# Kernel tuning notes

Hardware: AMD Instinct MI355X
Metric: run time of the kernel (lower is better)

Reference implementation:

```python
import jax, jax.numpy as jnp
import numpy as np

N = 50000      # nodes
IN = 128       # in_channels
H = 2          # heads
C = 64         # hidden_channels (per head)
E = 800000     # edges (before self-loops)
OUT = 40       # out_channels
BN_EPS = 1e-5
NEG_SLOPE = 0.2  # PyG GATConv default


def _bn(x, g, b):
    # BatchNorm1d forward with batch statistics (training-mode math, biased var)
    mu = jnp.mean(x, axis=0)
    v = jnp.var(x, axis=0)
    return (x - mu) * jax.lax.rsqrt(v + BN_EPS) * g + b


def _gat_conv(x, src, dst, W, a_src, a_dst, bias, concat):
    n = x.shape[0]
    h = (x @ W).reshape(n, H, C)                      # [N,H,C] per-head projection
    al_s = jnp.einsum('nhc,hc->nh', h, a_src)         # [N,H]
    al_d = jnp.einsum('nhc,hc->nh', h, a_dst)
    e = jax.nn.leaky_relu(al_s[src] + al_d[dst], NEG_SLOPE)  # [E,H]
    # segment softmax over edges sharing the same destination
    m = jax.ops.segment_max(e, dst, num_segments=n)
    ex = jnp.exp(e - m[dst])
    s = jax.ops.segment_sum(ex, dst, num_segments=n)
    alpha = ex / s[dst]                               # [E,H]
    out = jax.ops.segment_sum(h[src] * alpha[..., None], dst, num_segments=n)  # [N,H,C]
    out = out.reshape(n, H * C) if concat else out.mean(axis=1)
    return out + bias


def setup_inputs() -> dict:
    key = jax.random.key(0)
    ks = jax.random.split(key, 16)
    g = lambda k, shp, scale=1.0: jax.random.normal(k, shp, dtype=jnp.float32) * scale
    x = g(ks[0], (N, IN))
    edge_index = jax.random.randint(ks[1], (2, E), 0, N, dtype=jnp.int32)
    s = 1.0 / np.sqrt(IN)
    s2 = 1.0 / np.sqrt(H * C)
    return {
        'x': x,
        'edge_index': edge_index,
        'bn0_g': jnp.ones((IN,), jnp.float32), 'bn0_b': jnp.zeros((IN,), jnp.float32),
        'W1': g(ks[2], (IN, H * C), s), 'a1_src': g(ks[3], (H, C), s), 'a1_dst': g(ks[4], (H, C), s),
        'b1': jnp.zeros((H * C,), jnp.float32),
        'bn1_g': jnp.ones((H * C,), jnp.float32), 'bn1_b': jnp.zeros((H * C,), jnp.float32),
        'W2': g(ks[5], (H * C, H * C), s2), 'a2_src': g(ks[6], (H, C), s2), 'a2_dst': g(ks[7], (H, C), s2),
        'b2': jnp.zeros((C,), jnp.float32),
        'bn2_g': jnp.ones((C,), jnp.float32), 'bn2_b': jnp.zeros((C,), jnp.float32),
        'Wf': g(ks[8], (C, OUT), 1.0 / np.sqrt(C)), 'bf': jnp.zeros((OUT,), jnp.float32),
    }


def reference(x, edge_index, bn0_g, bn0_b, W1, a1_src, a1_dst, b1, bn1_g, bn1_b,
              W2, a2_src, a2_dst, b2, bn2_g, bn2_b, Wf, bf):
    n = x.shape[0]
    loop = jnp.arange(n, dtype=edge_index.dtype)
    src = jnp.concatenate([edge_index[0], loop])  # add self-loops (PyG default)
    dst = jnp.concatenate([edge_index[1], loop])
    h = _bn(x, bn0_g, bn0_b)
    # layer 1: concat heads
    h = _gat_conv(h, src, dst, W1, a1_src, a1_dst, b1, concat=True)
    h = jax.nn.elu(_bn(h, bn1_g, bn1_b))
    # (dropout is identity in eval mode)
    # layer 2: average heads
    h = _gat_conv(h, src, dst, W2, a2_src, a2_dst, b2, concat=False)
    h = jax.nn.elu(_bn(h, bn2_g, bn2_b))
    return h @ Wf + bf
```

## Files before the change

kernel.cpp:

```cpp
#include <hip/hip_runtime.h>
#include <hip/hip_fp16.h>


#define NEG_SLOPE 0.2f
#define BN_EPS 1e-5f

typedef short bf16x8 __attribute__((ext_vector_type(8)));
typedef float f32x4 __attribute__((ext_vector_type(4)));

static __device__ __forceinline__ unsigned short f2bf(float f) {
    union { float f; unsigned u; } v; v.f = f;
    unsigned r = v.u + 0x7FFF + ((v.u >> 16) & 1);
    return (unsigned short)(r >> 16);
}
static __device__ __forceinline__ float2 bf2x2(unsigned v) {
    union { unsigned u; float f; } a, b;
    a.u = v << 16; b.u = v & 0xffff0000u;
    return make_float2(a.f, b.f);
}
static __device__ __forceinline__ float halfsel(unsigned p, int head) {
    __half2 h = *(__half2*)&p;
    return head ? __high2float(h) : __low2float(h);
}

template <int C>
static __device__ __forceinline__ void d_bnstat(const float* __restrict__ x, int M,
                                                int rowsPerBlock, float* __restrict__ sums,
                                                int b, float* red) {
    constexpr int TPR = C / 4;
    constexpr int RS  = 256 / TPR;
    const int t = threadIdx.x;
    const int cg = t % TPR, rg = t / TPR, w = t >> 6, lane = t & 63;
    int r0 = b * rowsPerBlock + rg;
    int r1 = min(M, b * rowsPerBlock + rowsPerBlock);
    float4 s = make_float4(0, 0, 0, 0), q = make_float4(0, 0, 0, 0);
    #pragma unroll 4
    for (int r = r0; r < r1; r += RS) {
        float4 v = *(const float4*)&x[(size_t)r * C + cg * 4];
        s.x += v.x; s.y += v.y; s.z += v.z; s.w += v.w;
        q.x += v.x * v.x; q.y += v.y * v.y; q.z += v.z * v.z; q.w += v.w * v.w;
    }
    #pragma unroll
    for (int off = TPR; off < 64; off <<= 1) {
        s.x += __shfl_xor(s.x, off); s.y += __shfl_xor(s.y, off);
        s.z += __shfl_xor(s.z, off); s.w += __shfl_xor(s.w, off);
        q.x += __shfl_xor(q.x, off); q.y += __shfl_xor(q.y, off);
        q.z += __shfl_xor(q.z, off); q.w += __shfl_xor(q.w, off);
    }
    if (lane < TPR) {
        *(float4*)&red[w * 2 * C + cg * 4] = s;
        *(float4*)&red[w * 2 * C + C + cg * 4] = q;
    }
    __syncthreads();
    for (int idx = t; idx < 2 * C; idx += 256) {
        float tot = red[idx] + red[2 * C + idx] + red[4 * C + idx] + red[6 * C + idx];
        atomicAdd(&sums[idx], tot);
    }
}

template <int C>
__global__ __launch_bounds__(256) void k_bnstat2(const float* __restrict__ x, int M,
                                                 int rowsPerBlock, float* __restrict__ sums) {
    __shared__ __align__(16) float red[4 * 2 * C];
    d_bnstat<C>(x, M, rowsPerBlock, sums, blockIdx.x, red);
}

__global__ __launch_bounds__(256) void k_prep(
    const int* __restrict__ ei, int E, int rgrid,
    const float* __restrict__ x, int M, int bgrid,
    const float* __restrict__ W1, const float* __restrict__ W2,
    int* __restrict__ cnt, unsigned short* __restrict__ rank,
    float* __restrict__ sums,
    unsigned short* __restrict__ wt1, unsigned short* __restrict__ wt2) {
    __shared__ __align__(16) float red[4 * 2 * 128];
    int b = blockIdx.x;
    if (b < rgrid) {
        int i = b * 256 + threadIdx.x;
        if (i < E) {
            int d = ei[E + i];
            rank[i] = (unsigned short)atomicAdd(&cnt[d], 1);
        }
    } else if (b < rgrid + bgrid) {
        d_bnstat<128>(x, M, 256, sums, b - rgrid, red);
    } else {
        int idx = (b - rgrid - bgrid) * 256 + threadIdx.x;
        if (idx < 128 * 128) {
            int n = idx >> 7, k = idx & 127;
            wt1[idx] = f2bf(W1[k * 128 + n]);
            wt2[idx] = f2bf(W2[k * 128 + n]);
        }
    }
}

__global__ __launch_bounds__(256) void k_scan(const int* __restrict__ cnt, int Nn,
                                              int* __restrict__ gcur,
                                              int* __restrict__ rowptr,
                                              unsigned short* __restrict__ degs) {
    __shared__ int wsum[4];
    __shared__ int s_base;
    int t = threadIdx.x, lane = t & 63, w = t >> 6;
    int i = blockIdx.x * 256 + t;
    int v = (i < Nn) ? cnt[i] + 1 : 0;
    int x = v;
    #pragma unroll
    for (int off = 1; off < 64; off <<= 1) {
        int y = __shfl_up(x, off);
        if (lane >= off) x += y;
    }
    if (lane == 63) wsum[w] = x;
    __syncthreads();
    if (t < 4) {
        int val = wsum[t];
        int xs = val;
        #pragma unroll
        for (int off = 1; off < 4; off <<= 1) {
            int y = __shfl_up(xs, off);
            if (t >= off) xs += y;
        }
        if (t == 3) s_base = atomicAdd(gcur, xs);
        wsum[t] = xs - val;
    }
    __syncthreads();
    if (i < Nn) {
        rowptr[i] = s_base + wsum[w] + (x - v);
        degs[i] = (unsigned short)v;
    }
}

static __device__ __forceinline__ void d_fill(int b, const int* __restrict__ ei,
                                              const unsigned short* __restrict__ rank,
                                              const int* __restrict__ rowptr, int E, int Nn,
                                              unsigned short* __restrict__ ssrc) {
    int i = b * 256 + threadIdx.x;
    if (i < E) {
        int s = ei[i], d = ei[E + i];
        ssrc[rowptr[d] + 1 + (int)rank[i]] = (unsigned short)s;
    } else if (i < E + Nn) {
        int d = i - E;
        ssrc[rowptr[d]] = (unsigned short)d;
    }
}

static __device__ __forceinline__ void d_mfma(
    int blk, const float* __restrict__ A, const unsigned short* __restrict__ wt,
    const float* __restrict__ sums, const float* __restrict__ bng, const float* __restrict__ bnb,
    int elu, const float* __restrict__ asrc, const float* __restrict__ adst, int M,
    unsigned short* __restrict__ hb, float* __restrict__ als, float* __restrict__ ald) {
    __shared__ unsigned short As[64 * 136];
    __shared__ __align__(16) float stl[256];
    const int t = threadIdx.x;
    const int w = t >> 6, lane = t & 63;
    const int c = lane & 15, q = lane >> 4;
    const int row0 = blk * 64;

    if (t < 128) {
        float mu = sums[t] / (float)M;
        float var = sums[128 + t] / (float)M - mu * mu;
        float s = bng[t] * rsqrtf(var + BN_EPS);
        stl[t] = s;
        stl[128 + t] = bnb[t] - mu * s;
    }
    __syncthreads();

    const int gr = row0 + w * 16 + c;
    const bool rok = gr < M;

    float4 av[4][2];
    #pragma unroll
    for (int ks = 0; ks < 4; ks++) {
        const int cc = (ks * 4 + q) * 8;
        #pragma unroll
        for (int h = 0; h < 2; h++)
            av[ks][h] = rok ? *(const float4*)&A[(size_t)gr * 128 + cc + h * 4]
                            : make_float4(0.f, 0.f, 0.f, 0.f);
    }

    bf16x8 af[4];
    #pragma unroll
    for (int ks = 0; ks < 4; ks++) {
        const int cc = (ks * 4 + q) * 8;
        union { bf16x8 v; unsigned u[4]; } pk;
        #pragma unroll
        for (int h = 0; h < 2; h++) {
            float4 v = av[ks][h];
            if (rok) {
                float4 sc = *(const float4*)&stl[cc + h * 4];
                float4 sh = *(const float4*)&stl[128 + cc + h * 4];
                v.x = v.x * sc.x + sh.x; v.y = v.y * sc.y + sh.y;
                v.z = v.z * sc.z + sh.z; v.w = v.w * sc.w + sh.w;
                if (elu) {
                    v.x = v.x > 0.f ? v.x : expm1f(v.x);
                    v.y = v.y > 0.f ? v.y : expm1f(v.y);
                    v.z = v.z > 0.f ? v.z : expm1f(v.z);
                    v.w = v.w > 0.f ? v.w : expm1f(v.w);
                }
            }
            pk.u[h * 2]     = ((unsigned)f2bf(v.y) << 16) | f2bf(v.x);
            pk.u[h * 2 + 1] = ((unsigned)f2bf(v.w) << 16) | f2bf(v.z);
        }
        af[ks] = pk.v;
    }

    f32x4 acc[8] = {};
    #pragma unroll
    for (int half = 0; half < 2; half++) {
        bf16x8 br[8][2];
        #pragma unroll
        for (int tl = 0; tl < 8; tl++) {
            #pragma unroll
            for (int kk = 0; kk < 2; kk++)
                br[tl][kk] = *(const bf16x8*)&wt[(size_t)(tl * 16 + c) * 128 + ((half * 2 + kk) * 4 + q) * 8];
        }
        #pragma unroll
        for (int kk = 0; kk < 2; kk++) {
            #pragma unroll
            for (int tl = 0; tl < 8; tl++)
                acc[tl] = __builtin_amdgcn_mfma_f32_16x16x32_bf16(af[half * 2 + kk], br[tl][kk], acc[tl], 0, 0, 0);
        }
    }

    float as_[8], ad_[8];
    #pragma unroll
    for (int tl = 0; tl < 8; tl++) { as_[tl] = asrc[tl * 16 + c]; ad_[tl] = adst[tl * 16 + c]; }
    #pragma unroll
    for (int reg = 0; reg < 4; reg++) {
        float s0 = 0.f, s1 = 0.f, d0 = 0.f, d1 = 0.f;
        #pragma unroll
        for (int tl = 0; tl < 4; tl++) { s0 += acc[tl][reg] * as_[tl]; d0 += acc[tl][reg] * ad_[tl]; }
        #pragma unroll
        for (int tl = 4; tl < 8; tl++) { s1 += acc[tl][reg] * as_[tl]; d1 += acc[tl][reg] * ad_[tl]; }
        #pragma unroll
        for (int off = 1; off < 16; off <<= 1) {
            s0 += __shfl_xor(s0, off); s1 += __shfl_xor(s1, off);
            d0 += __shfl_xor(d0, off); d1 += __shfl_xor(d1, off);
        }
        int grow = row0 + w * 16 + q * 4 + reg;
        if (c == 0 && grow < M) {
            *(float2*)&als[(size_t)grow * 2] = make_float2(s0, s1);
            *(float2*)&ald[(size_t)grow * 2] = make_float2(d0, d1);
        }
    }

    #pragma unroll
    for (int reg = 0; reg < 4; reg++) {
        #pragma unroll
        for (int tl = 0; tl < 8; tl++)
            As[(w * 16 + q * 4 + reg) * 136 + tl * 16 + c] = f2bf(acc[tl][reg]);
    }
    #pragma unroll
    for (int j = 0; j < 4; j++) {
        int f = j * 64 + lane;
        int r = f >> 4, ch = f & 15;
        int grow = row0 + w * 16 + r;
        if (grow < M) {
            uint4 v = *(uint4*)&As[(w * 16 + r) * 136 + ch * 8];
            *(uint4*)&hb[(size_t)grow * 128 + ch * 8] = v;
        }
    }
}

__global__ __launch_bounds__(256) void k_mfma(
    const float* __restrict__ A, const unsigned short* __restrict__ wt,
    const float* __restrict__ sums, const float* __restrict__ bng, const float* __restrict__ bnb,
    int elu, const float* __restrict__ asrc, const float* __restrict__ adst, int M,
    unsigned short* __restrict__ hb, float* __restrict__ als, float* __restrict__ ald) {
    d_mfma(blockIdx.x, A, wt, sums, bng, bnb, elu, asrc, adst, M, hb, als, ald);
}

__global__ __launch_bounds__(256) void k_fill_mfma(
    const float* __restrict__ A, const unsigned short* __restrict__ wt,
    const float* __restrict__ sums, const float* __restrict__ bng, const float* __restrict__ bnb,
    const float* __restrict__ asrc, const float* __restrict__ adst, int M, int ggrid,
    unsigned short* __restrict__ hb, float* __restrict__ als, float* __restrict__ ald,
    const int* __restrict__ ei, const unsigned short* __restrict__ rank,
    const int* __restrict__ rowptr, int E, int Nn, unsigned short* __restrict__ ssrc) {
    if (blockIdx.x < ggrid)
        d_mfma(blockIdx.x, A, wt, sums, bng, bnb, 0, asrc, adst, M, hb, als, ald);
    else
        d_fill(blockIdx.x - ggrid, ei, rank, rowptr, E, Nn, ssrc);
}

static __device__ __forceinline__ void acc8(float* acc, uint4 v, float a) {
    float2 p;
    p = bf2x2(v.x); acc[0] += a * p.x; acc[1] += a * p.y;
    p = bf2x2(v.y); acc[2] += a * p.x; acc[3] += a * p.y;
    p = bf2x2(v.z); acc[4] += a * p.x; acc[5] += a * p.y;
    p = bf2x2(v.w); acc[6] += a * p.x; acc[7] += a * p.y;
}

template <int MEAN>
static __device__ __forceinline__ void attnagg(
    const int* __restrict__ rowptr, const unsigned short* __restrict__ degs,
    const unsigned short* __restrict__ ssrc,
    const float* __restrict__ als, const float* __restrict__ ald,
    float* __restrict__ alpha, const unsigned short* __restrict__ hb,
    const float* __restrict__ bias, int Nn, float* __restrict__ out) {
    int gw = (blockIdx.x * blockDim.x + threadIdx.x) >> 6;
    if (gw >= Nn) return;
    int lane = threadIdx.x & 63;
    int sub = lane >> 4, c = lane & 15, head = c >> 3;
    int beg = rowptr[gw];
    int deg = (int)degs[gw];
    int end = beg + deg;
    float2 dv = *(const float2*)&ald[(size_t)gw * 2];
    float acc[8] = {};

    if (deg <= 64) {
        bool on = lane < deg;
        int eidx = beg + (on ? lane : 0);
        int sreg = (int)ssrc[eidx];
        float2 av = *(const float2*)&als[(size_t)sreg * 2];
        float v0 = av.x + dv.x; v0 = v0 > 0.f ? v0 : NEG_SLOPE * v0;
        float v1 = av.y + dv.y; v1 = v1 > 0.f ? v1 : NEG_SLOPE * v1;
        float p0 = on ? __expf(v0) : 0.f;
        float p1 = on ? __expf(v1) : 0.f;
        float t0 = p0, t1 = p1;
        #pragma unroll
        for (int off = 32; off; off >>= 1) {
            t0 += __shfl_xor(t0, off);
            t1 += __shfl_xor(t1, off);
        }
        __half2 hpk = __floats2half2_rn(p0 / t0, p1 / t1);
        unsigned pk = *(unsigned*)&hpk;

        int nit = (deg + 3) >> 2;
        int it = 0;
        for (; it + 4 <= nit; it += 4) {
            int s_[4]; float a_[4];
            #pragma unroll
            for (int u = 0; u < 4; u++) {
                int jj = (it + u) * 4 + sub;
                int ls = jj & 63;
                s_[u] = __shfl(sreg, ls);
                unsigned pw = (unsigned)__shfl(pk, ls);
                a_[u] = (jj < deg) ? halfsel(pw, head) : 0.f;
            }
            #pragma unroll
            for (int u = 0; u < 4; u++) {
                uint4 v = *(const uint4*)&hb[(size_t)s_[u] * 128 + c * 8];
                acc8(acc, v, a_[u]);
            }
        }
        for (; it < nit; it += 2) {
            const bool two = (it + 1) < nit;
            int s_[2]; float a_[2];
            #pragma unroll
            for (int u = 0; u < 2; u++) {
                if (u == 0 || two) {
                    int jj = (it + u) * 4 + sub;
                    int ls = jj & 63;
                    s_[u] = __shfl(sreg, ls);
                    unsigned pw = (unsigned)__shfl(pk, ls);
                    a_[u] = (jj < deg) ? halfsel(pw, head) : 0.f;
                }
            }
            #pragma unroll
            for (int u = 0; u < 2; u++) {
                if (u == 0 || two) {
                    uint4 v = *(const uint4*)&hb[(size_t)s_[u] * 128 + c * 8];
                    acc8(acc, v, a_[u]);
                }
            }
        }
    } else {
        float d0 = dv.x, d1 = dv.y;
        float m0 = -1e30f, m1 = -1e30f;
        for (int e = beg + lane; e < end; e += 64) {
            int s = (int)ssrc[e];
            float v0 = als[s * 2] + d0;     v0 = v0 > 0.f ? v0 : NEG_SLOPE * v0;
            float v1 = als[s * 2 + 1] + d1; v1 = v1 > 0.f ? v1 : NEG_SLOPE * v1;
            m0 = fmaxf(m0, v0); m1 = fmaxf(m1, v1);
        }
        #pragma unroll
        for (int off = 32; off; off >>= 1) {
            m0 = fmaxf(m0, __shfl_xor(m0, off));
            m1 = fmaxf(m1, __shfl_xor(m1, off));
        }
        float t0 = 0.f, t1 = 0.f;
        for (int e = beg + lane; e < end; e += 64) {
            int s = (int)ssrc[e];
            float v0 = als[s * 2] + d0;     v0 = v0 > 0.f ? v0 : NEG_SLOPE * v0;
            float v1 = als[s * 2 + 1] + d1; v1 = v1 > 0.f ? v1 : NEG_SLOPE * v1;
            float p0 = __expf(v0 - m0), p1 = __expf(v1 - m1);
            alpha[e * 2] = p0; alpha[e * 2 + 1] = p1;
            t0 += p0; t1 += p1;
        }
        #pragma unroll
        for (int off = 32; off; off >>= 1) {
            t0 += __shfl_xor(t0, off);
            t1 += __shfl_xor(t1, off);
        }
        float i0 = 1.f / t0, i1 = 1.f / t1;
        for (int e = beg + sub; e < end; e += 4) {
            int s = (int)ssrc[e];
            float a = (head ? alpha[(size_t)e * 2 + 1] * i1 : alpha[(size_t)e * 2] * i0);
            uint4 v = *(const uint4*)&hb[(size_t)s * 128 + c * 8];
            acc8(acc, v, a);
        }
    }

    #pragma unroll
    for (int j2 = 0; j2 < 8; j2++) {
        acc[j2] += __shfl_xor(acc[j2], 16);
        acc[j2] += __shfl_xor(acc[j2], 32);
        if (MEAN) acc[j2] += __shfl_xor(acc[j2], 8);
    }
    if (MEAN) {
        if (sub == 0 && c < 8) {
            float4 b0 = *(const float4*)&bias[c * 8];
            float4 b1 = *(const float4*)&bias[c * 8 + 4];
            float4 o0 = make_float4(0.5f * acc[0] + b0.x, 0.5f * acc[1] + b0.y, 0.5f * acc[2] + b0.z, 0.5f * acc[3] + b0.w);
            float4 o1 = make_float4(0.5f * acc[4] + b1.x, 0.5f * acc[5] + b1.y, 0.5f * acc[6] + b1.z, 0.5f * acc[7] + b1.w);
            *(float4*)&out[(size_t)gw * 64 + c * 8] = o0;
            *(float4*)&out[(size_t)gw * 64 + c * 8 + 4] = o1;
        }
    } else {
        if (sub == 0) {
            float4 b0 = *(const float4*)&bias[c * 8];
            float4 b1 = *(const float4*)&bias[c * 8 + 4];
            float4 o0 = make_float4(acc[0] + b0.x, acc[1] + b0.y, acc[2] + b0.z, acc[3] + b0.w);
            float4 o1 = make_float4(acc[4] + b1.x, acc[5] + b1.y, acc[6] + b1.z, acc[7] + b1.w);
            *(float4*)&out[(size_t)gw * 128 + c * 8] = o0;
            *(float4*)&out[(size_t)gw * 128 + c * 8 + 4] = o1;
        }
    }
}

__global__ __launch_bounds__(256) void k_attnagg1(const int* __restrict__ rowptr, const unsigned short* __restrict__ degs,
                                                  const unsigned short* __restrict__ ssrc,
                                                  const float* __restrict__ als, const float* __restrict__ ald,
                                                  float* __restrict__ alpha, const unsigned short* __restrict__ hb,
                                                  const float* __restrict__ bias, int Nn, float* __restrict__ out) {
    attnagg<0>(rowptr, degs, ssrc, als, ald, alpha, hb, bias, Nn, out);
}

__global__ __launch_bounds__(256) void k_attnagg2(const int* __restrict__ rowptr, const unsigned short* __restrict__ degs,
                                                  const unsigned short* __restrict__ ssrc,
                                                  const float* __restrict__ als, const float* __restrict__ ald,
                                                  float* __restrict__ alpha, const unsigned short* __restrict__ hb,
                                                  const float* __restrict__ bias, int Nn, float* __restrict__ out) {
    attnagg<1>(rowptr, degs, ssrc, als, ald, alpha, hb, bias, Nn, out);
}

__global__ __launch_bounds__(128) void k_gemmf(const float* __restrict__ A, const float* __restrict__ Wf,
                                               const float* __restrict__ bf,
                                               const float* __restrict__ sums, const float* __restrict__ bng,
                                               const float* __restrict__ bnb,
                                               int M, float* __restrict__ out) {
    __shared__ float As[128 * 65];
    __shared__ float Bs[64 * 40];
    __shared__ float stl[128];
    int t = threadIdx.x;
    int row0 = blockIdx.x * 128;
    if (t < 64) {
        float mu = sums[t] / (float)M;
        float var = sums[64 + t] / (float)M - mu * mu;
        float s = bng[t] * rsqrtf(var + BN_EPS);
        stl[t] = s;
        stl[64 + t] = bnb[t] - mu * s;
    }
    __syncthreads();
    for (int i = t; i < 64 * 40; i += 128) Bs[i] = Wf[i];
    for (int i = t; i < 128 * 64; i += 128) {
        int r = i >> 6, k = i & 63;
        int gr = row0 + r;
        float v = 0.f;
        if (gr < M) {
            v = A[(size_t)gr * 64 + k] * stl[k] + stl[64 + k];
            v = v > 0.f ? v : expm1f(v);
        }
        As[r * 65 + k] = v;
    }
    __syncthreads();
    int cg = t & 3, rg = t >> 2;
    float acc[4][10] = {};
    for (int k = 0; k < 64; k++) {
        float b[10];
        #pragma unroll
        for (int j = 0; j < 10; j++) b[j] = Bs[k * 40 + cg * 10 + j];
        #pragma unroll
        for (int r = 0; r < 4; r++) {
            float a = As[(rg * 4 + r) * 65 + k];
            #pragma unroll
            for (int j = 0; j < 10; j++) acc[r][j] += a * b[j];
        }
    }
    for (int r = 0; r < 4; r++) {
        int gr = row0 + rg * 4 + r;
        if (gr < M) {
            #pragma unroll
            for (int j = 0; j < 10; j++) out[(size_t)gr * 40 + cg * 10 + j] = acc[r][j] + bf[cg * 10 + j];
        }
    }
}

extern "C" void kernel_launch(void* const* d_in, const int* in_sizes, int n_in,
                              void* d_out, int out_size, void* d_ws, size_t ws_size,
                              hipStream_t stream) {
    const float* x     = (const float*)d_in[0];
    const int*   ei    = (const int*)d_in[1];
    const float* bn0_g = (const float*)d_in[2];
    const float* bn0_b = (const float*)d_in[3];
    const float* W1    = (const float*)d_in[4];
    const float* a1s   = (const float*)d_in[5];
    const float* a1d   = (const float*)d_in[6];
    const float* b1    = (const float*)d_in[7];
    const float* bn1_g = (const float*)d_in[8];
    const float* bn1_b = (const float*)d_in[9];
    const float* W2    = (const float*)d_in[10];
    const float* a2s   = (const float*)d_in[11];
    const float* a2d   = (const float*)d_in[12];
    const float* b2    = (const float*)d_in[13];
    const float* bn2_g = (const float*)d_in[14];
    const float* bn2_b = (const float*)d_in[15];
    const float* Wf    = (const float*)d_in[16];
    const float* bf    = (const float*)d_in[17];
    float* out = (float*)d_out;

    const int N  = in_sizes[0] / 128;
    const int E  = in_sizes[1] / 2;
    const int ET = E + N;

    char* ws = (char*)d_ws;
    size_t off = 0;
    auto alloc = [&](size_t bytes) -> char* {
        char* p = ws + off;
        off = (off + bytes + 255) & ~(size_t)255;
        return p;
    };
    float* sums   = (float*)alloc(644 * 4);
    int*   gcur   = (int*)(sums + 640);
    int*   cnt    = (int*)alloc((size_t)N * 4);
    const size_t zlen = off;
    int*   rowptr = (int*)alloc((size_t)N * 4);
    unsigned short* degs = (unsigned short*)alloc((size_t)N * 2);
    unsigned short* ssrc = (unsigned short*)alloc((size_t)ET * 2);
    unsigned short* rank = (unsigned short*)alloc((size_t)E * 2);
    float* abuf   = (float*)alloc((size_t)N * 128 * 4);
    unsigned short* hb  = (unsigned short*)alloc((size_t)N * 128 * 2);
    unsigned short* wt1 = (unsigned short*)alloc((size_t)128 * 128 * 2);
    unsigned short* wt2 = (unsigned short*)alloc((size_t)128 * 128 * 2);
    float* alpha  = (float*)alloc((size_t)ET * 2 * 4);
    float* als    = (float*)alloc((size_t)N * 2 * 4);
    float* ald    = (float*)alloc((size_t)N * 2 * 4);

    const int tb = 256;
    const int rgrid = (E + tb - 1) / tb;
    const int bgrid = (N + 255) / 256;
    const int fgrid = (ET + tb - 1) / tb;
    const int wgrid = ((size_t)N * 64 + tb - 1) / tb;
    const int ggrid = (N + 63) / 64;

    hipMemsetAsync(ws, 0, zlen, stream);

    k_prep<<<rgrid + bgrid + 64, tb, 0, stream>>>(ei, E, rgrid, x, N, bgrid, W1, W2,
                                                  cnt, rank, sums, wt1, wt2);
    k_scan<<<bgrid, tb, 0, stream>>>(cnt, N, gcur, rowptr, degs);

    k_fill_mfma<<<ggrid + fgrid, tb, 0, stream>>>(x, wt1, sums, bn0_g, bn0_b,
                                                  a1s, a1d, N, ggrid, hb, als, ald,
                                                  ei, rank, rowptr, E, N, ssrc);
    k_attnagg1<<<wgrid, tb, 0, stream>>>(rowptr, degs, ssrc, als, ald, alpha, hb, b1, N, abuf);

    k_bnstat2<128><<<bgrid, 256, 0, stream>>>(abuf, N, 256, sums + 256);

    k_mfma<<<ggrid, tb, 0, stream>>>(abuf, wt2, sums + 256, bn1_g, bn1_b, 1, a2s, a2d, N, hb, als, ald);
    k_attnagg2<<<wgrid, tb, 0, stream>>>(rowptr, degs, ssrc, als, ald, alpha, hb, b2, N, abuf);

    k_bnstat2<64><<<bgrid, 256, 0, stream>>>(abuf, N, 256, sums + 512);

    k_gemmf<<<(N + 127) / 128, 128, 0, stream>>>(abuf, Wf, bf, sums + 512, bn2_g, bn2_b, N, out);
}
```

Measured before the change: 332.6 us.

## Reschedule CSR build, overlap rank atomics with first GEMM, stage GEMM tiles in LDS

Moves the per-edge rank atomics out of the prep kernel and interleaves them, as odd blocks, with the layer-1 MFMA GEMM blocks so the atomic-bound and compute-bound work overlap. Scan and fill become separate launches that run after it. The GEMM now stages the normalized A tile and the full bf16 weight matrix in shared memory and writes hb directly from the accumulators. BN-stat grids use 64 rows per block for more parallelism. The costs are an extra launch, a larger LDS footprint that can lower occupancy, and scattered 2-byte hb stores.

```diff
diff --git a/kernel.cpp b/kernel.cpp
--- a/kernel.cpp
+++ b/kernel.cpp
@@ -34,7 +34,7 @@
     int r0 = b * rowsPerBlock + rg;
     int r1 = min(M, b * rowsPerBlock + rowsPerBlock);
     float4 s = make_float4(0, 0, 0, 0), q = make_float4(0, 0, 0, 0);
-    #pragma unroll 4
+    #pragma unroll
     for (int r = r0; r < r1; r += RS) {
         float4 v = *(const float4*)&x[(size_t)r * C + cg * 4];
         s.x += v.x; s.y += v.y; s.z += v.z; s.w += v.w;
@@ -65,25 +65,17 @@
     d_bnstat<C>(x, M, rowsPerBlock, sums, blockIdx.x, red);
 }
 
-__global__ __launch_bounds__(256) void k_prep(
-    const int* __restrict__ ei, int E, int rgrid,
+__global__ __launch_bounds__(256) void k_pre(
     const float* __restrict__ x, int M, int bgrid,
     const float* __restrict__ W1, const float* __restrict__ W2,
-    int* __restrict__ cnt, unsigned short* __restrict__ rank,
     float* __restrict__ sums,
     unsigned short* __restrict__ wt1, unsigned short* __restrict__ wt2) {
     __shared__ __align__(16) float red[4 * 2 * 128];
     int b = blockIdx.x;
-    if (b < rgrid) {
-        int i = b * 256 + threadIdx.x;
-        if (i < E) {
-            int d = ei[E + i];
-            rank[i] = (unsigned short)atomicAdd(&cnt[d], 1);
-        }
-    } else if (b < rgrid + bgrid) {
-        d_bnstat<128>(x, M, 256, sums, b - rgrid, red);
+    if (b < bgrid) {
+        d_bnstat<128>(x, M, 64, sums, b, red);
     } else {
-        int idx = (b - rgrid - bgrid) * 256 + threadIdx.x;
+        int idx = (b - bgrid) * 256 + threadIdx.x;
         if (idx < 128 * 128) {
             int n = idx >> 7, k = idx & 127;
             wt1[idx] = f2bf(W1[k * 128 + n]);
@@ -127,11 +119,11 @@
     }
 }
 
-static __device__ __forceinline__ void d_fill(int b, const int* __restrict__ ei,
+__global__ __launch_bounds__(256) void k_fill(const int* __restrict__ ei,
                                               const unsigned short* __restrict__ rank,
                                               const int* __restrict__ rowptr, int E, int Nn,
                                               unsigned short* __restrict__ ssrc) {
-    int i = b * 256 + threadIdx.x;
+    int i = blockIdx.x * 256 + threadIdx.x;
     if (i < E) {
         int s = ei[i], d = ei[E + i];
         ssrc[rowptr[d] + 1 + (int)rank[i]] = (unsigned short)s;
@@ -147,6 +139,7 @@
     int elu, const float* __restrict__ asrc, const float* __restrict__ adst, int M,
     unsigned short* __restrict__ hb, float* __restrict__ als, float* __restrict__ ald) {
     __shared__ unsigned short As[64 * 136];
+    __shared__ unsigned short Bs[128 * 136];
     __shared__ __align__(16) float stl[256];
     const int t = threadIdx.x;
     const int w = t >> 6, lane = t & 63;
@@ -162,60 +155,55 @@
     }
     __syncthreads();
 
-    const int gr = row0 + w * 16 + c;
-    const bool rok = gr < M;
-
-    float4 av[4][2];
+    #pragma unroll
+    for (int i = 0; i < 8; i++) {
+        int idx = t + i * 256;
+        int r = idx >> 5, ch4 = idx & 31;
+        int gr = row0 + r;
+        float4 v = make_float4(0, 0, 0, 0);
+        if (gr < M) {
+            v = *(const float4*)&A[(size_t)gr * 128 + ch4 * 4];
+            float4 sc = *(const float4*)&stl[ch4 * 4];
+            float4 sh = *(const float4*)&stl[128 + ch4 * 4];
+            v.x = v.x * sc.x + sh.x; v.y = v.y * sc.y + sh.y;
+            v.z = v.z * sc.z + sh.z; v.w = v.w * sc.w + sh.w;
+            if (elu) {
+                v.x = v.x > 0.f ? v.x : expm1f(v.x);
+                v.y = v.y > 0.f ? v.y : expm1f(v.y);
+                v.z = v.z > 0.f ? v.z : expm1f(v.z);
+                v.w = v.w > 0.f ? v.w : expm1f(v.w);
+            }
+        }
+        unsigned p0 = ((unsigned)f2bf(v.y) << 16) | f2bf(v.x);
+        unsigned p1 = ((unsigned)f2bf(v.w) << 16) | f2bf(v.z);
+        *(uint2*)&As[r * 136 + ch4 * 4] = make_uint2(p0, p1);
+    }
+    #pragma unroll
+    for (int i = 0; i < 8; i++) {
+        int idx = t + i * 256;
+        int r = idx >> 4, ch = idx & 15;
+        *(uint4*)&Bs[r * 136 + ch * 8] = *(const uint4*)&wt[(size_t)r * 128 + ch * 8];
+    }
+    __syncthreads();
+
+    f32x4 acc[8] = {};
     #pragma unroll
     for (int ks = 0; ks < 4; ks++) {
-        const int cc = (ks * 4 + q) * 8;
-        #pragma unroll
-        for (int h = 0; h < 2; h++)
-            av[ks][h] = rok ? *(const float4*)&A[(size_t)gr * 128 + cc + h * 4]
-                            : make_float4(0.f, 0.f, 0.f, 0.f);
-    }
-
-    bf16x8 af[4];
-    #pragma unroll
-    for (int ks = 0; ks < 4; ks++) {
-        const int cc = (ks * 4 + q) * 8;
-        union { bf16x8 v; unsigned u[4]; } pk;
-        #pragma unroll
-        for (int h = 0; h < 2; h++) {
-            float4 v = av[ks][h];
-            if (rok) {
-                float4 sc = *(const float4*)&stl[cc + h * 4];
-                float4 sh = *(const float4*)&stl[128 + cc + h * 4];
-                v.x = v.x * sc.x + sh.x; v.y = v.y * sc.y + sh.y;
-                v.z = v.z * sc.z + sh.z; v.w = v.w * sc.w + sh.w;
-                if (elu) {
-                    v.x = v.x > 0.f ? v.x : expm1f(v.x);
-                    v.y = v.y > 0.f ? v.y : expm1f(v.y);
-                    v.z = v.z > 0.f ? v.z : expm1f(v.z);
-                    v.w = v.w > 0.f ? v.w : expm1f(v.w);
-                }
-            }
-            pk.u[h * 2]     = ((unsigned)f2bf(v.y) << 16) | f2bf(v.x);
-            pk.u[h * 2 + 1] = ((unsigned)f2bf(v.w) << 16) | f2bf(v.z);
-        }
-        af[ks] = pk.v;
-    }
-
-    f32x4 acc[8] = {};
-    #pragma unroll
-    for (int half = 0; half < 2; half++) {
-        bf16x8 br[8][2];
+        bf16x8 a = *(bf16x8*)&As[(w * 16 + c) * 136 + (ks * 4 + q) * 8];
         #pragma unroll
         for (int tl = 0; tl < 8; tl++) {
-            #pragma unroll
-            for (int kk = 0; kk < 2; kk++)
-                br[tl][kk] = *(const bf16x8*)&wt[(size_t)(tl * 16 + c) * 128 + ((half * 2 + kk) * 4 + q) * 8];
-        }
-        #pragma unroll
-        for (int kk = 0; kk < 2; kk++) {
+            bf16x8 b = *(bf16x8*)&Bs[(tl * 16 + c) * 136 + (ks * 4 + q) * 8];
+            acc[tl] = __builtin_amdgcn_mfma_f32_16x16x32_bf16(a, b, acc[tl], 0, 0, 0);
+        }
+    }
+
+    #pragma unroll
+    for (int reg = 0; reg < 4; reg++) {
+        int grow = row0 + w * 16 + q * 4 + reg;
+        if (grow < M) {
             #pragma unroll
             for (int tl = 0; tl < 8; tl++)
-                acc[tl] = __builtin_amdgcn_mfma_f32_16x16x32_bf16(af[half * 2 + kk], br[tl][kk], acc[tl], 0, 0, 0);
+                hb[(size_t)grow * 128 + tl * 16 + c] = f2bf(acc[tl][reg]);
         }
     }
 
@@ -238,23 +226,6 @@
         if (c == 0 && grow < M) {
             *(float2*)&als[(size_t)grow * 2] = make_float2(s0, s1);
             *(float2*)&ald[(size_t)grow * 2] = make_float2(d0, d1);
-        }
-    }
-
-    #pragma unroll
-    for (int reg = 0; reg < 4; reg++) {
-        #pragma unroll
-        for (int tl = 0; tl < 8; tl++)
-            As[(w * 16 + q * 4 + reg) * 136 + tl * 16 + c] = f2bf(acc[tl][reg]);
-    }
-    #pragma unroll
-    for (int j = 0; j < 4; j++) {
-        int f = j * 64 + lane;
-        int r = f >> 4, ch = f & 15;
-        int grow = row0 + w * 16 + r;
-        if (grow < M) {
-            uint4 v = *(uint4*)&As[(w * 16 + r) * 136 + ch * 8];
-            *(uint4*)&hb[(size_t)grow * 128 + ch * 8] = v;
         }
     }
 }
@@ -267,17 +238,27 @@
     d_mfma(blockIdx.x, A, wt, sums, bng, bnb, elu, asrc, adst, M, hb, als, ald);
 }
 
-__global__ __launch_bounds__(256) void k_fill_mfma(
+__global__ __launch_bounds__(256) void k_rank_mfma(
     const float* __restrict__ A, const unsigned short* __restrict__ wt,
     const float* __restrict__ sums, const float* __restrict__ bng, const float* __restrict__ bnb,
     const float* __restrict__ asrc, const float* __restrict__ adst, int M, int ggrid,
     unsigned short* __restrict__ hb, float* __restrict__ als, float* __restrict__ ald,
-    const int* __restrict__ ei, const unsigned short* __restrict__ rank,
-    const int* __restrict__ rowptr, int E, int Nn, unsigned short* __restrict__ ssrc) {
-    if (blockIdx.x < ggrid)
-        d_mfma(blockIdx.x, A, wt, sums, bng, bnb, 0, asrc, adst, M, hb, als, ald);
-    else
-        d_fill(blockIdx.x - ggrid, ei, rank, rowptr, E, Nn, ssrc);
+    const int* __restrict__ ei, int E, int rblocks, int chunk,
+    int* __restrict__ cnt, unsigned short* __restrict__ rank) {
+    int b = blockIdx.x;
+    int half = b >> 1;
+    if ((b & 1) == 0) {
+        if (half < ggrid)
+            d_mfma(half, A, wt, sums, bng, bnb, 0, asrc, adst, M, hb, als, ald);
+    } else {
+        if (half < rblocks) {
+            int i1 = min(E, half * chunk + chunk);
+            for (int i = half * chunk + threadIdx.x; i < i1; i += 256) {
+                int d = ei[E + i];
+                rank[i] = (unsigned short)atomicAdd(&cnt[d], 1);
+            }
+        }
+    }
 }
 
 static __device__ __forceinline__ void acc8(float* acc, uint4 v, float a) {
@@ -545,29 +526,34 @@
     float* ald    = (float*)alloc((size_t)N * 2 * 4);
 
     const int tb = 256;
-    const int rgrid = (E + tb - 1) / tb;
-    const int bgrid = (N + 255) / 256;
+    const int bgrid0 = (N + 63) / 64;
+    const int sgrid = (N + 255) / 256;
     const int fgrid = (ET + tb - 1) / tb;
     const int wgrid = ((size_t)N * 64 + tb - 1) / tb;
     const int ggrid = (N + 63) / 64;
+    const int rblocks = ggrid;
+    const int chunk = (E + rblocks - 1) / rblocks;
 
     hipMemsetAsync(ws, 0, zlen, stream);
 
-    k_prep<<<rgrid + bgrid + 64, tb, 0, stream>>>(ei, E, rgrid, x, N, bgrid, W1, W2,
-                                                  cnt, rank, sums, wt1, wt2);
-    k_scan<<<bgrid, tb, 0, stream>>>(cnt, N, gcur, rowptr, degs);
-
-    k_fill_mfma<<<ggrid + fgrid, tb, 0, stream>>>(x, wt1, sums, bn0_g, bn0_b,
-                                                  a1s, a1d, N, ggrid, hb, als, ald,
-                                                  ei, rank, rowptr, E, N, ssrc);
+    k_pre<<<bgrid0 + 64, tb, 0, stream>>>(x, N, bgrid0, W1, W2, sums, wt1, wt2);
+
+    k_rank_mfma<<<2 * ggrid, tb, 0, stream>>>(x, wt1, sums, bn0_g, bn0_b,
+                                              a1s, a1d, N, ggrid, hb, als, ald,
+                                              ei, E, rblocks, chunk, cnt, rank);
+
+    k_scan<<<sgrid, tb, 0, stream>>>(cnt, N, gcur, rowptr, degs);
+
+    k_fill<<<fgrid, tb, 0, stream>>>(ei, rank, rowptr, E, N, ssrc);
+
     k_attnagg1<<<wgrid, tb, 0, stream>>>(rowptr, degs, ssrc, als, ald, alpha, hb, b1, N, abuf);
 
-    k_bnstat2<128><<<bgrid, 256, 0, stream>>>(abuf, N, 256, sums + 256);
+    k_bnstat2<128><<<bgrid0, 256, 0, stream>>>(abuf, N, 64, sums + 256);
 
     k_mfma<<<ggrid, tb, 0, stream>>>(abuf, wt2, sums + 256, bn1_g, bn1_b, 1, a2s, a2d, N, hb, als, ald);
     k_attnagg2<<<wgrid, tb, 0, stream>>>(rowptr, degs, ssrc, als, ald, alpha, hb, b2, N, abuf);
 
-    k_bnstat2<64><<<bgrid, 256, 0, stream>>>(abuf, N, 256, sums + 512);
+    k_bnstat2<64><<<bgrid0, 256, 0, stream>>>(abuf, N, 64, sums + 512);
 
     k_gemmf<<<(N + 127) / 128, 128, 0, stream>>>(abuf, Wf, bf, sums + 512, bn2_g, bn2_b, N, out);
 }
```

Measured after the change: 358.4 us. +7.8%, slower.

## Split GEMM block into 32-row tiles with per-head wave partition via LDS A staging

Applied to the files above, without the earlier changes.

The fused BN/ELU + bf16 MFMA projection kernel now processes 32 rows per block instead of 64. Each wave handles 16 rows and one head (64 output columns), so it needs only 4 accumulators instead of 8. The A tile is normalized, converted to bf16 and staged cooperatively through shared memory with coalesced loads. Output goes straight to global as scalar bf16 stores rather than through an LDS transpose. The intent is to cut register pressure and double the grid for better occupancy, at the cost of reading the weight matrix twice as often and issuing narrower, less coalesced hb stores.

```diff
diff --git a/kernel.cpp b/kernel.cpp
--- a/kernel.cpp
+++ b/kernel.cpp
@@ -146,12 +146,13 @@
     const float* __restrict__ sums, const float* __restrict__ bng, const float* __restrict__ bnb,
     int elu, const float* __restrict__ asrc, const float* __restrict__ adst, int M,
     unsigned short* __restrict__ hb, float* __restrict__ als, float* __restrict__ ald) {
-    __shared__ unsigned short As[64 * 136];
+    __shared__ unsigned short As[32 * 136];
     __shared__ __align__(16) float stl[256];
     const int t = threadIdx.x;
     const int w = t >> 6, lane = t & 63;
     const int c = lane & 15, q = lane >> 4;
-    const int row0 = blk * 64;
+    const int rw = w & 1, h = w >> 1;
+    const int row0 = blk * 32;
 
     if (t < 128) {
         float mu = sums[t] / (float)M;
@@ -162,99 +163,71 @@
     }
     __syncthreads();
 
-    const int gr = row0 + w * 16 + c;
-    const bool rok = gr < M;
-
-    float4 av[4][2];
+    #pragma unroll
+    for (int i = 0; i < 4; i++) {
+        int idx = t + i * 256;
+        int r = idx >> 5, ch4 = idx & 31;
+        int gr = row0 + r;
+        float4 v = make_float4(0, 0, 0, 0);
+        if (gr < M) {
+            v = *(const float4*)&A[(size_t)gr * 128 + ch4 * 4];
+            float4 sc = *(const float4*)&stl[ch4 * 4];
+            float4 sh = *(const float4*)&stl[128 + ch4 * 4];
+            v.x = v.x * sc.x + sh.x; v.y = v.y * sc.y + sh.y;
+            v.z = v.z * sc.z + sh.z; v.w = v.w * sc.w + sh.w;
+            if (elu) {
+                v.x = v.x > 0.f ? v.x : expm1f(v.x);
+                v.y = v.y > 0.f ? v.y : expm1f(v.y);
+                v.z = v.z > 0.f ? v.z : expm1f(v.z);
+                v.w = v.w > 0.f ? v.w : expm1f(v.w);
+            }
+        }
+        unsigned p0 = ((unsigned)f2bf(v.y) << 16) | f2bf(v.x);
+        unsigned p1 = ((unsigned)f2bf(v.w) << 16) | f2bf(v.z);
+        *(uint2*)&As[r * 136 + ch4 * 4] = make_uint2(p0, p1);
+    }
+    __syncthreads();
+
+    f32x4 acc[4] = {};
     #pragma unroll
     for (int ks = 0; ks < 4; ks++) {
-        const int cc = (ks * 4 + q) * 8;
-        #pragma unroll
-        for (int h = 0; h < 2; h++)
-            av[ks][h] = rok ? *(const float4*)&A[(size_t)gr * 128 + cc + h * 4]
-                            : make_float4(0.f, 0.f, 0.f, 0.f);
-    }
-
-    bf16x8 af[4];
-    #pragma unroll
-    for (int ks = 0; ks < 4; ks++) {
-        const int cc = (ks * 4 + q) * 8;
-        union { bf16x8 v; unsigned u[4]; } pk;
-        #pragma unroll
-        for (int h = 0; h < 2; h++) {
-            float4 v = av[ks][h];
-            if (rok) {
-                float4 sc = *(const float4*)&stl[cc + h * 4];
-                float4 sh = *(const float4*)&stl[128 + cc + h * 4];
-                v.x = v.x * sc.x + sh.x; v.y = v.y * sc.y + sh.y;
-                v.z = v.z * sc.z + sh.z; v.w = v.w * sc.w + sh.w;
-                if (elu) {
-                    v.x = v.x > 0.f ? v.x : expm1f(v.x);
-                    v.y = v.y > 0.f ? v.y : expm1f(v.y);
-                    v.z = v.z > 0.f ? v.z : expm1f(v.z);
-                    v.w = v.w > 0.f ? v.w : expm1f(v.w);
-                }
-            }
-            pk.u[h * 2]     = ((unsigned)f2bf(v.y) << 16) | f2bf(v.x);
-            pk.u[h * 2 + 1] = ((unsigned)f2bf(v.w) << 16) | f2bf(v.z);
-        }
-        af[ks] = pk.v;
-    }
-
-    f32x4 acc[8] = {};
-    #pragma unroll
-    for (int half = 0; half < 2; half++) {
-        bf16x8 br[8][2];
-        #pragma unroll
-        for (int tl = 0; tl < 8; tl++) {
-            #pragma unroll
-            for (int kk = 0; kk < 2; kk++)
-                br[tl][kk] = *(const bf16x8*)&wt[(size_t)(tl * 16 + c) * 128 + ((half * 2 + kk) * 4 + q) * 8];
-        }
-        #pragma unroll
-        for (int kk = 0; kk < 2; kk++) {
-            #pragma unroll
-            for (int tl = 0; tl < 8; tl++)
-                acc[tl] = __builtin_amdgcn_mfma_f32_16x16x32_bf16(af[half * 2 + kk], br[tl][kk], acc[tl], 0, 0, 0);
-        }
-    }
-
-    float as_[8], ad_[8];
-    #pragma unroll
-    for (int tl = 0; tl < 8; tl++) { as_[tl] = asrc[tl * 16 + c]; ad_[tl] = adst[tl * 16 + c]; }
+        bf16x8 a = *(bf16x8*)&As[(rw * 16 + c) * 136 + (ks * 4 + q) * 8];
+        #pragma unroll
+        for (int tl = 0; tl < 4; tl++) {
+            bf16x8 b = *(const bf16x8*)&wt[(size_t)((h * 4 + tl) * 16 + c) * 128 + (ks * 4 + q) * 8];
+            acc[tl] = __builtin_amdgcn_mfma_f32_16x16x32_bf16(a, b, acc[tl], 0, 0, 0);
+        }
+    }
+
     #pragma unroll
     for (int reg = 0; reg < 4; reg++) {
-        float s0 = 0.f, s1 = 0.f, d0 = 0.f, d1 = 0.f;
-        #pragma unroll
-        for (int tl = 0; tl < 4; tl++) { s0 += acc[tl][reg] * as_[tl]; d0 += acc[tl][reg] * ad_[tl]; }
-        #pragma unroll
-        for (int tl = 4; tl < 8; tl++) { s1 += acc[tl][reg] * as_[tl]; d1 += acc[tl][reg] * ad_[tl]; }
+        int grow = row0 + rw * 16 + q * 4 + reg;
+        if (grow < M) {
+            #pragma unroll
+            for (int tl = 0; tl < 4; tl++)
+                hb[(size_t)grow * 128 + h * 64 + tl * 16 + c] = f2bf(acc[tl][reg]);
+        }
+    }
+
+    float as_[4], ad_[4];
+    #pragma unroll
+    for (int tl = 0; tl < 4; tl++) {
+        as_[tl] = asrc[h * 64 + tl * 16 + c];
+        ad_[tl] = adst[h * 64 + tl * 16 + c];
+    }
+    #pragma unroll
+    for (int reg = 0; reg < 4; reg++) {
+        float s = 0.f, d = 0.f;
+        #pragma unroll
+        for (int tl = 0; tl < 4; tl++) { s += acc[tl][reg] * as_[tl]; d += acc[tl][reg] * ad_[tl]; }
         #pragma unroll
         for (int off = 1; off < 16; off <<= 1) {
-            s0 += __shfl_xor(s0, off); s1 += __shfl_xor(s1, off);
-            d0 += __shfl_xor(d0, off); d1 += __shfl_xor(d1, off);
-        }
-        int grow = row0 + w * 16 + q * 4 + reg;
+            s += __shfl_xor(s, off); d += __shfl_xor(d, off);
+        }
+        int grow = row0 + rw * 16 + q * 4 + reg;
         if (c == 0 && grow < M) {
-            *(float2*)&als[(size_t)grow * 2] = make_float2(s0, s1);
-            *(float2*)&ald[(size_t)grow * 2] = make_float2(d0, d1);
-        }
-    }
-
-    #pragma unroll
-    for (int reg = 0; reg < 4; reg++) {
-        #pragma unroll
-        for (int tl = 0; tl < 8; tl++)
-            As[(w * 16 + q * 4 + reg) * 136 + tl * 16 + c] = f2bf(acc[tl][reg]);
-    }
-    #pragma unroll
-    for (int j = 0; j < 4; j++) {
-        int f = j * 64 + lane;
-        int r = f >> 4, ch = f & 15;
-        int grow = row0 + w * 16 + r;
-        if (grow < M) {
-            uint4 v = *(uint4*)&As[(w * 16 + r) * 136 + ch * 8];
-            *(uint4*)&hb[(size_t)grow * 128 + ch * 8] = v;
+            als[(size_t)grow * 2 + h] = s;
+            ald[(size_t)grow * 2 + h] = d;
         }
     }
 }
@@ -549,7 +522,7 @@
     const int bgrid = (N + 255) / 256;
     const int fgrid = (ET + tb - 1) / tb;
     const int wgrid = ((size_t)N * 64 + tb - 1) / tb;
-    const int ggrid = (N + 63) / 64;
+    const int ggrid = (N + 31) / 32;
 
     hipMemsetAsync(ws, 0, zlen, stream);
 
```

Result: faster. 323.0 us (-2.9%).
